# Optimization experiments

Measured on AMD Instinct MI355X. Metric: run time of the kernel, lower is better.

Reference implementation:

```python
import jax, jax.numpy as jnp
import numpy as np


def _lstm_dir(x, w_ih, w_hh, b, reverse):
    # x: [S,B,I], w_ih: [4H,I], w_hh: [4H,H], b: [4H]. torch gate order i,f,g,o.
    H = w_hh.shape[1]
    gx = jnp.einsum('sbi,gi->sbg', x, w_ih) + b  # precompute input projections
    B = x.shape[1]
    h0 = jnp.zeros((B, H), x.dtype)

    def step(carry, g):
        h, c = carry
        z = g + h @ w_hh.T
        i, f, gg, o = jnp.split(z, 4, axis=-1)
        c = jax.nn.sigmoid(f) * c + jax.nn.sigmoid(i) * jnp.tanh(gg)
        h = jax.nn.sigmoid(o) * jnp.tanh(c)
        return (h, c), h

    (hT, _), hs = jax.lax.scan(step, (h0, h0), gx, reverse=reverse)
    return hs, hT  # hs: [S,B,H] in original time order; hT final hidden


def _bilstm_layer(x, w_ih, w_hh, b):
    # x: [S,B,I]; params stacked [2, ...] for (forward, backward)
    hs_f, hT_f = _lstm_dir(x, w_ih[0], w_hh[0], b[0], reverse=False)
    hs_b, hT_b = _lstm_dir(x, w_ih[1], w_hh[1], b[1], reverse=True)
    return jnp.concatenate([hs_f, hs_b], axis=-1), hT_f, hT_b


def reference(tokens, emb, w_ih0, w_hh0, b0, w_ih1, w_hh1, b1, fc1_w, fc1_b, fc2_w, fc2_b):
    # tokens: [B,S] int; embedding lookup (frozen table)
    x = emb[tokens]                       # [B,S,E]
    x = jnp.transpose(x, (1, 0, 2))       # [S,B,E] time-major for scan
    h0_seq, _, _ = _bilstm_layer(x, w_ih0, w_hh0, b0)          # [S,B,2H]
    _, hT_f, hT_b = _bilstm_layer(h0_seq, w_ih1, w_hh1, b1)    # final layer
    out = jnp.concatenate([hT_f, hT_b], axis=-1)               # [B,2H]
    out = jax.nn.relu(out @ fc1_w.T + fc1_b)
    return out @ fc2_w.T + fc2_b          # [B,2]


def setup_inputs() -> dict:
    key = jax.random.key(0)
    ks = jax.random.split(key, 13)
    B, S, V, E, H = 256, 512, 50000, 300, 128
    s = 0.05
    return {
        'tokens': jax.random.randint(ks[0], (B, S), 0, V, dtype=jnp.int32),
        'emb':    jax.random.normal(ks[1], (V, E), jnp.float32) * s,
        'w_ih0':  jax.random.normal(ks[2], (2, 4 * H, E), jnp.float32) * s,
        'w_hh0':  jax.random.normal(ks[3], (2, 4 * H, H), jnp.float32) * s,
        'b0':     jax.random.normal(ks[4], (2, 4 * H), jnp.float32) * s,
        'w_ih1':  jax.random.normal(ks[5], (2, 4 * H, 2 * H), jnp.float32) * s,
        'w_hh1':  jax.random.normal(ks[6], (2, 4 * H, H), jnp.float32) * s,
        'b1':     jax.random.normal(ks[7], (2, 4 * H), jnp.float32) * s,
        'fc1_w':  jax.random.normal(ks[8], (H, 2 * H), jnp.float32) * s,
        'fc1_b':  jax.random.normal(ks[9], (H,), jnp.float32) * s,
        'fc2_w':  jax.random.normal(ks[10], (2, H), jnp.float32) * s,
        'fc2_b':  jax.random.normal(ks[11], (2,), jnp.float32) * s,
    }
```

## Files before the change

### kernel.cpp

```cpp
#include <hip/hip_runtime.h>

#define S_LEN 512
#define BATCH 256
#define EMB_D 300
#define EMB_PAD 320
#define HID 128
#define SB (S_LEN*BATCH)
#define CH 128
#define NCH 4
#define GXC_DIR ((size_t)CH*BATCH*512)
#define SMEM_BYTES 86016

typedef __attribute__((ext_vector_type(8))) short bf16x8;
typedef __attribute__((ext_vector_type(4))) float f32x4;
typedef unsigned short u16;
typedef unsigned int   u32;

__device__ __forceinline__ float b2f(u16 u) {
    union { u32 i; float f; } v; v.i = ((u32)u) << 16; return v.f;
}
__device__ __forceinline__ u16 f2b(float f) {
    union { float f; u32 i; } v; v.f = f;
    u32 r = v.i + 0x7fffu + ((v.i >> 16) & 1u);
    return (u16)(r >> 16);
}
__device__ __forceinline__ float sigf(float x) {
    return __builtin_amdgcn_rcpf(1.f + __expf(-x));
}
__device__ __forceinline__ float tanhf_fast(float x) {
    float e = __expf(2.f * x);
    return 1.f - 2.f * __builtin_amdgcn_rcpf(e + 1.f);
}

__global__ void k_detect(const u16* __restrict__ emb_u, int* __restrict__ flag) {
    __shared__ int cnt;
    if (threadIdx.x == 0) cnt = 0;
    __syncthreads();
    float v = b2f(emb_u[2 * threadIdx.x + 64]);
    float a = fabsf(v);
    if (a > 1e-4f && a < 16.f) atomicAdd(&cnt, 1);
    __syncthreads();
    if (threadIdx.x == 0) *flag = (cnt > 128) ? 1 : 0;
}

__global__ void k_packw(const void* __restrict__ src, u16* __restrict__ dst,
                        int Kin, int Kpad, int total, const int* __restrict__ flag) {
    int i = blockIdx.x * 256 + threadIdx.x;
    if (i >= total) return;
    int n = i / Kpad, k = i - n * Kpad;
    int d = n >> 9, r = n & 511, j = r >> 2, t = r & 3;
    size_t si = (size_t)((d << 9) + (t << 7) + j) * Kin + k;
    u16 v = 0;
    if (k < Kin) {
        if (*flag) v = ((const u16*)src)[si];
        else       v = f2b(((const float*)src)[si]);
    }
    dst[i] = v;
}

__global__ void k_packb(const void* __restrict__ src, float* __restrict__ dst,
                        const int* __restrict__ flag) {
    int i = blockIdx.x * 256 + threadIdx.x;
    if (i >= 1024) return;
    int d = i >> 9, r = i & 511, j = r >> 2, t = r & 3;
    size_t si = (d << 9) + (t << 7) + j;
    dst[i] = (*flag) ? b2f(((const u16*)src)[si]) : ((const float*)src)[si];
}

template<int KPAD, bool EMBED, bool IS_L0>
__global__ __launch_bounds__(1024) void k_fused(
    const int* __restrict__ tok, const void* __restrict__ Asrc,
    const u16* __restrict__ W, const float* __restrict__ bias,
    u16* __restrict__ gx_out, const u16* __restrict__ gx_in,
    const u16* __restrict__ Whp,
    u16* __restrict__ h0seq, float* __restrict__ hT,
    u16* __restrict__ hstate, float* __restrict__ cstate,
    int k, int nlstm, int soff0g, int soff1g, const int* __restrict__ flag)
{
    __shared__ __align__(16) char smem[SMEM_BYTES];
    const int tid = threadIdx.x;

    if ((int)blockIdx.x < nlstm) {
        u16* hb = (u16*)smem;
        u16* gb = (u16*)(smem + 8704);
        const int d    = blockIdx.x >> 4;
        const int bg   = blockIdx.x & 15;
        const int wv   = tid >> 6, lane = tid & 63, quad = lane >> 4, col = lane & 15;
        const int soff = (d == 0) ? CH * k : CH * (NCH - 1 - k);

        for (int i = tid; i < 2 * 16 * 136; i += 1024) hb[i] = 0;
        __syncthreads();
        if (k > 0) {
            for (int i = tid; i < 16 * 128; i += 1024) {
                int bl = i >> 7, j = i & 127;
                hb[bl * 136 + j] = hstate[((size_t)d * BATCH + bg * 16 + bl) * 128 + j];
            }
        }

        const u16* Wd = Whp + (size_t)d * 512 * 128;
        bf16x8 wf[2][4];
#pragma unroll
        for (int mt = 0; mt < 2; ++mt)
#pragma unroll
            for (int ks = 0; ks < 4; ++ks)
                wf[mt][ks] = *(const bf16x8*)(Wd + (size_t)(((wv * 2 + mt) * 16) + col) * 128 + ks * 32 + quad * 8);

        const u16* gxd = gx_in + (size_t)d * GXC_DIR;
        auto sloc = [&](int si) { return (d == 0) ? si : (CH - 1 - si); };
        auto prefetch = [&](int si, int P) {
            const u16* g0 = gxd + ((size_t)sloc(si) * BATCH + bg * 16 + wv) * 512 + lane * 8;
            __builtin_amdgcn_global_load_lds((const __attribute__((address_space(1))) void*)g0,
                (__attribute__((address_space(3))) void*)(gb + (P * 16 + wv) * 520), 16, 0, 0);
        };

        float c[2];
#pragma unroll
        for (int mt = 0; mt < 2; ++mt)
            c[mt] = (k > 0) ? cstate[((size_t)d * BATCH + bg * 16 + col) * 128 + (wv * 2 + mt) * 4 + quad] : 0.f;

        auto step = [&](int si, int P) {
            if (si + 1 < CH) prefetch(si + 1, P ^ 1);
            if constexpr (IS_L0) {
                if (si > 0) {
                    int sp = soff + ((d == 0) ? (si - 1) : (CH - si));
                    ushort2 hv = *(const ushort2*)(hb + (P * 16 + wv) * 136 + lane * 2);
                    *(ushort2*)(h0seq + ((size_t)sp * BATCH + bg * 16 + wv) * 256 + (d << 7) + lane * 2) = hv;
                }
            }
            bf16x8 hf[4];
#pragma unroll
            for (int ks = 0; ks < 4; ++ks)
                hf[ks] = *(const bf16x8*)(hb + (P * 16 + col) * 136 + ks * 32 + quad * 8);
            f32x4 z[2];
#pragma unroll
            for (int mt = 0; mt < 2; ++mt) {
                ushort4 gv = *(const ushort4*)(gb + (P * 16 + col) * 520 + (wv * 2 + mt) * 16 + quad * 4);
                z[mt][0] = b2f(gv.x); z[mt][1] = b2f(gv.y); z[mt][2] = b2f(gv.z); z[mt][3] = b2f(gv.w);
            }
#pragma unroll
            for (int ks = 0; ks < 4; ++ks)
#pragma unroll
                for (int mt = 0; mt < 2; ++mt)
                    z[mt] = __builtin_amdgcn_mfma_f32_16x16x32_bf16(wf[mt][ks], hf[ks], z[mt], 0, 0, 0);
#pragma unroll
            for (int mt = 0; mt < 2; ++mt) {
                float iv = sigf(z[mt][0]), fv = sigf(z[mt][1]);
                float gg = tanhf_fast(z[mt][2]), ov = sigf(z[mt][3]);
                c[mt] = fv * c[mt] + iv * gg;
                float hv = ov * tanhf_fast(c[mt]);
                const int j = (wv * 2 + mt) * 4 + quad;
                hb[((P ^ 1) * 16 + col) * 136 + j] = f2b(hv);
                if constexpr (!IS_L0) {
                    if (k == NCH - 1 && si == CH - 1)
                        hT[((size_t)d * BATCH + bg * 16 + col) * 128 + j] = hv;
                }
            }
            __syncthreads();
        };

        prefetch(0, 0);
        __syncthreads();

        for (int si = 0; si < CH; si += 2) {
            step(si, 0);
            step(si + 1, 1);
        }

        if constexpr (IS_L0) {
            int sp = soff + ((d == 0) ? (CH - 1) : 0);
            ushort2 hv = *(const ushort2*)(hb + wv * 136 + lane * 2);
            *(ushort2*)(h0seq + ((size_t)sp * BATCH + bg * 16 + wv) * 256 + (d << 7) + lane * 2) = hv;
        }
        if (k < NCH - 1) {
            for (int i = tid; i < 16 * 128; i += 1024) {
                int bl = i >> 7, j = i & 127;
                hstate[((size_t)d * BATCH + bg * 16 + bl) * 128 + j] = hb[bl * 136 + j];
            }
#pragma unroll
            for (int mt = 0; mt < 2; ++mt)
                cstate[((size_t)d * BATCH + bg * 16 + col) * 128 + (wv * 2 + mt) * 4 + quad] = c[mt];
        }
        return;
    }

    const int g   = (int)blockIdx.x - nlstm;
    u16* As = (u16*)smem;
    u16* Bs = (u16*)(smem + 10240);
    const int gy  = g >> 8;
    const int m0  = (g & 255) * 128;
    const int dir = gy >> 2;
    const int n0  = (gy & 3) * 128;
    const int soff = dir ? soff1g : soff0g;
    const size_t mg0 = (size_t)soff * BATCH;
    const int w = tid >> 6, lane = tid & 63, quad = lane >> 4, l16 = lane & 15;
    const int wm = w >> 2, wn = w & 3;
    const int crow = (tid & 511) >> 2, cseg = tid & 3;
    const bool isA = tid < 512;

    bool is_bf = true;
    size_t arow_off = 0;
    const u16* brow = nullptr;
    if (isA) {
        if constexpr (EMBED) {
            size_t m = mg0 + m0 + crow;
            int s = (int)(m >> 8), b = (int)(m & 255);
            is_bf = (*flag != 0);
            arow_off = (size_t)tok[b * S_LEN + s] * EMB_D;
        } else {
            arow_off = (mg0 + m0 + crow) * KPAD;
        }
    } else {
        brow = W + (size_t)(dir * 512 + n0 + crow) * KPAD;
    }

    f32x4 acc[2][2] = {};
    const int KSTEPS = KPAD / 32;
#pragma unroll
    for (int kk = 0; kk < KSTEPS; ++kk) {
        uint4 v;
        if (isA) {
            if constexpr (EMBED) {
                u32 u[4];
                if (is_bf) {
                    const u16* ar = (const u16*)Asrc + arow_off;
#pragma unroll
                    for (int i = 0; i < 4; ++i) {
                        int cc = kk * 32 + cseg * 8 + 2 * i;
                        u[i] = (cc < EMB_D) ? *(const u32*)(ar + cc) : 0u;
                    }
                } else {
                    const float* ar = (const float*)Asrc + arow_off;
#pragma unroll
                    for (int i = 0; i < 4; ++i) {
                        int cc = kk * 32 + cseg * 8 + 2 * i;
                        if (cc < EMB_D) {
                            float2 f = *(const float2*)(ar + cc);
                            u[i] = (u32)f2b(f.x) | ((u32)f2b(f.y) << 16);
                        } else u[i] = 0u;
                    }
                }
                v.x = u[0]; v.y = u[1]; v.z = u[2]; v.w = u[3];
            } else {
                v = *((const uint4*)((const u16*)Asrc + arow_off) + kk * 4 + cseg);
            }
        } else {
            v = *((const uint4*)brow + kk * 4 + cseg);
        }
        __syncthreads();
        if (isA) *(uint4*)(As + crow * 40 + cseg * 8) = v;
        else     *(uint4*)(Bs + crow * 40 + cseg * 8) = v;
        __syncthreads();
        bf16x8 af[2], bfr[2];
#pragma unroll
        for (int mt = 0; mt < 2; ++mt)
            af[mt] = *(const bf16x8*)(As + (wm * 32 + mt * 16 + l16) * 40 + quad * 8);
#pragma unroll
        for (int nt = 0; nt < 2; ++nt)
            bfr[nt] = *(const bf16x8*)(Bs + (wn * 32 + nt * 16 + l16) * 40 + quad * 8);
#pragma unroll
        for (int mt = 0; mt < 2; ++mt)
#pragma unroll
            for (int nt = 0; nt < 2; ++nt)
                acc[mt][nt] = __builtin_amdgcn_mfma_f32_16x16x32_bf16(af[mt], bfr[nt], acc[mt][nt], 0, 0, 0);
    }
#pragma unroll
    for (int mt = 0; mt < 2; ++mt)
#pragma unroll
        for (int nt = 0; nt < 2; ++nt)
#pragma unroll
            for (int r = 0; r < 4; ++r) {
                int mloc = m0 + wm * 32 + mt * 16 + quad * 4 + r;
                int nloc = n0 + wn * 32 + nt * 16 + l16;
                float vv = acc[mt][nt][r] + bias[dir * 512 + nloc];
                gx_out[(size_t)dir * GXC_DIR + (size_t)mloc * 512 + nloc] = f2b(vv);
            }
}

__global__ void k_fc(const float* __restrict__ hT,
                     const void* __restrict__ fc1w, const void* __restrict__ fc1b,
                     const void* __restrict__ fc2w, const void* __restrict__ fc2b,
                     void* __restrict__ out, const int* __restrict__ flag) {
    int b = blockIdx.x, j = threadIdx.x;
    bool is_bf = (*flag != 0);
    __shared__ float u[128];
    float a = is_bf ? b2f(((const u16*)fc1b)[j]) : ((const float*)fc1b)[j];
    for (int k = 0; k < 256; ++k) {
        float x = hT[((size_t)(k >> 7) * BATCH + b) * 128 + (k & 127)];
        float w = is_bf ? b2f(((const u16*)fc1w)[j * 256 + k]) : ((const float*)fc1w)[j * 256 + k];
        a += x * w;
    }
    u[j] = fmaxf(a, 0.f);
    __syncthreads();
    if (j < 2) {
        float a2 = is_bf ? b2f(((const u16*)fc2b)[j]) : ((const float*)fc2b)[j];
        for (int q = 0; q < 128; ++q) {
            float w = is_bf ? b2f(((const u16*)fc2w)[j * 128 + q]) : ((const float*)fc2w)[j * 128 + q];
            a2 += u[q] * w;
        }
        if (is_bf) ((u16*)out)[b * 2 + j] = f2b(a2);
        else       ((float*)out)[b * 2 + j] = a2;
    }
}

extern "C" void kernel_launch(void* const* d_in, const int* in_sizes, int n_in,
                              void* d_out, int out_size, void* d_ws, size_t ws_size,
                              hipStream_t stream) {
    const int*  tok   = (const int*)d_in[0];
    const void* emb   = d_in[1];
    const void* w_ih0 = d_in[2];
    const void* w_hh0 = d_in[3];
    const void* b0    = d_in[4];
    const void* w_ih1 = d_in[5];
    const void* w_hh1 = d_in[6];
    const void* b1    = d_in[7];
    const void* fc1w  = d_in[8];
    const void* fc1b  = d_in[9];
    const void* fc2w  = d_in[10];
    const void* fc2b  = d_in[11];

    char* ws = (char*)d_ws;
    size_t off = 0;
    auto alloc = [&](size_t bytes) -> void* {
        void* p = ws + off; off += (bytes + 255) & ~(size_t)255; return p;
    };
    int*   flag   = (int*)alloc(256);
    u16*   Wp0    = (u16*)alloc(1024 * 320 * 2);
    u16*   Wp1    = (u16*)alloc(1024 * 256 * 2);
    u16*   Whp0   = (u16*)alloc(1024 * 128 * 2);
    u16*   Whp1   = (u16*)alloc(1024 * 128 * 2);
    float* bp0    = (float*)alloc(1024 * 4);
    float* bp1    = (float*)alloc(1024 * 4);
    float* hT     = (float*)alloc((size_t)2 * BATCH * 128 * 4);
    u16*   hstate = (u16*)alloc((size_t)2 * BATCH * 128 * 2);
    float* cstate = (float*)alloc((size_t)2 * BATCH * 128 * 4);
    u16*   h0seq  = (u16*)alloc((size_t)SB * 256 * 2);
    size_t bufb   = 2 * GXC_DIR * sizeof(u16);
    u16*   gxcA   = (u16*)alloc(bufb);
    bool overlap  = ws_size >= off + bufb;
    u16*   gxcB   = overlap ? (u16*)alloc(bufb) : gxcA;

    k_detect<<<1, 256, 0, stream>>>((const u16*)emb, flag);

    k_packw<<<(1024 * 320 + 255) / 256, 256, 0, stream>>>(w_ih0, Wp0, 300, 320, 1024 * 320, flag);
    k_packw<<<(1024 * 256 + 255) / 256, 256, 0, stream>>>(w_ih1, Wp1, 256, 256, 1024 * 256, flag);
    k_packw<<<(1024 * 128 + 255) / 256, 256, 0, stream>>>(w_hh0, Whp0, 128, 128, 1024 * 128, flag);
    k_packw<<<(1024 * 128 + 255) / 256, 256, 0, stream>>>(w_hh1, Whp1, 128, 128, 1024 * 128, flag);
    k_packb<<<4, 256, 0, stream>>>(b0, bp0, flag);
    k_packb<<<4, 256, 0, stream>>>(b1, bp1, flag);

    const int NG = 2048;

    if (overlap) {
        k_fused<320, true, true><<<NG, 1024, 0, stream>>>(
            tok, emb, Wp0, bp0, gxcA, gxcA, Whp0, h0seq, nullptr, hstate, cstate,
            0, 0, 0, CH * (NCH - 1), flag);
        for (int k = 0; k < NCH; ++k) {
            int ng = (k < NCH - 1) ? NG : 0;
            u16* gin  = (k & 1) ? gxcB : gxcA;
            u16* gout = (k & 1) ? gxcA : gxcB;
            k_fused<320, true, true><<<32 + ng, 1024, 0, stream>>>(
                tok, emb, Wp0, bp0, gout, gin, Whp0, h0seq, nullptr, hstate, cstate,
                k, 32, CH * (k + 1), CH * (NCH - 2 - k), flag);
        }
        k_fused<256, false, false><<<NG, 1024, 0, stream>>>(
            nullptr, h0seq, Wp1, bp1, gxcA, gxcA, Whp1, nullptr, hT, hstate, cstate,
            0, 0, 0, CH * (NCH - 1), flag);
        for (int k = 0; k < NCH; ++k) {
            int ng = (k < NCH - 1) ? NG : 0;
            u16* gin  = (k & 1) ? gxcB : gxcA;
            u16* gout = (k & 1) ? gxcA : gxcB;
            k_fused<256, false, false><<<32 + ng, 1024, 0, stream>>>(
                nullptr, h0seq, Wp1, bp1, gout, gin, Whp1, nullptr, hT, hstate, cstate,
                k, 32, CH * (k + 1), CH * (NCH - 2 - k), flag);
        }
    } else {
        for (int k = 0; k < NCH; ++k) {
            k_fused<320, true, true><<<NG, 1024, 0, stream>>>(
                tok, emb, Wp0, bp0, gxcA, gxcA, Whp0, h0seq, nullptr, hstate, cstate,
                0, 0, CH * k, CH * (NCH - 1 - k), flag);
            k_fused<320, true, true><<<32, 1024, 0, stream>>>(
                tok, emb, Wp0, bp0, gxcA, gxcA, Whp0, h0seq, nullptr, hstate, cstate,
                k, 32, 0, 0, flag);
        }
        for (int k = 0; k < NCH; ++k) {
            k_fused<256, false, false><<<NG, 1024, 0, stream>>>(
                nullptr, h0seq, Wp1, bp1, gxcA, gxcA, Whp1, nullptr, hT, hstate, cstate,
                0, 0, CH * k, CH * (NCH - 1 - k), flag);
            k_fused<256, false, false><<<32, 1024, 0, stream>>>(
                nullptr, h0seq, Wp1, bp1, gxcA, gxcA, Whp1, nullptr, hT, hstate, cstate,
                k, 32, 0, 0, flag);
        }
    }
    k_fc<<<256, 128, 0, stream>>>(hT, fc1w, fc1b, fc2w, fc2b, d_out, flag);
}
```

Before: 1.560 ms.

## Restructure input-projection GEMM to keep full-K A tile resident and loop over N

The input-projection GEMM blocks now load a 64-row A tile with the full K extent into shared memory once, then loop over eight 64-column slices of the weight matrix, each loaded with full K. Before, each block computed a 128x128 tile by streaming 32-wide K slices, with a sync pair per step. The goal is to reuse the gathered embedding rows across all 512 gate outputs and cut redundant gathers, halving the GEMM block count. The cost is fewer MFMAs per wave per tile (a single 16x16 accumulator), more shared-memory footprint, and an extra sync pair per N slice.

```diff
diff --git a/kernel.cpp b/kernel.cpp
--- a/kernel.cpp
+++ b/kernel.cpp
@@ -183,97 +183,76 @@
         return;
     }
 
-    const int g   = (int)blockIdx.x - nlstm;
+    const int g = (int)blockIdx.x - nlstm;
+    constexpr int KSTEPS = KPAD / 32;
+    constexpr int AST    = KPAD + 8;
+    constexpr int NCHK   = 64 * (KPAD / 8);
     u16* As = (u16*)smem;
-    u16* Bs = (u16*)(smem + 10240);
-    const int gy  = g >> 8;
-    const int m0  = (g & 255) * 128;
-    const int dir = gy >> 2;
-    const int n0  = (gy & 3) * 128;
+    u16* Bs = (u16*)(smem + (size_t)64 * AST * 2);
+    const int dir  = g >> 9;
+    const int m0   = (g & 511) * 64;
     const int soff = dir ? soff1g : soff0g;
     const size_t mg0 = (size_t)soff * BATCH;
     const int w = tid >> 6, lane = tid & 63, quad = lane >> 4, l16 = lane & 15;
     const int wm = w >> 2, wn = w & 3;
-    const int crow = (tid & 511) >> 2, cseg = tid & 3;
-    const bool isA = tid < 512;
-
-    bool is_bf = true;
-    size_t arow_off = 0;
-    const u16* brow = nullptr;
-    if (isA) {
+    const bool is_bf = EMBED ? (*flag != 0) : true;
+
+    for (int ch = tid; ch < NCHK; ch += 1024) {
+        int row = ch / (KPAD / 8), seg = ch % (KPAD / 8);
+        uint4 v;
         if constexpr (EMBED) {
-            size_t m = mg0 + m0 + crow;
+            u32 u[4];
+            size_t m = mg0 + m0 + row;
             int s = (int)(m >> 8), b = (int)(m & 255);
-            is_bf = (*flag != 0);
-            arow_off = (size_t)tok[b * S_LEN + s] * EMB_D;
+            size_t aro = (size_t)tok[b * S_LEN + s] * EMB_D;
+            if (is_bf) {
+                const u16* ar = (const u16*)Asrc + aro;
+#pragma unroll
+                for (int i = 0; i < 4; ++i) {
+                    int cc = seg * 8 + 2 * i;
+                    u[i] = (cc < EMB_D) ? *(const u32*)(ar + cc) : 0u;
+                }
+            } else {
+                const float* ar = (const float*)Asrc + aro;
+#pragma unroll
+                for (int i = 0; i < 4; ++i) {
+                    int cc = seg * 8 + 2 * i;
+                    if (cc < EMB_D) {
+                        float2 f = *(const float2*)(ar + cc);
+                        u[i] = (u32)f2b(f.x) | ((u32)f2b(f.y) << 16);
+                    } else u[i] = 0u;
+                }
+            }
+            v.x = u[0]; v.y = u[1]; v.z = u[2]; v.w = u[3];
         } else {
-            arow_off = (mg0 + m0 + crow) * KPAD;
-        }
-    } else {
-        brow = W + (size_t)(dir * 512 + n0 + crow) * KPAD;
-    }
-
-    f32x4 acc[2][2] = {};
-    const int KSTEPS = KPAD / 32;
-#pragma unroll
-    for (int kk = 0; kk < KSTEPS; ++kk) {
-        uint4 v;
-        if (isA) {
-            if constexpr (EMBED) {
-                u32 u[4];
-                if (is_bf) {
-                    const u16* ar = (const u16*)Asrc + arow_off;
-#pragma unroll
-                    for (int i = 0; i < 4; ++i) {
-                        int cc = kk * 32 + cseg * 8 + 2 * i;
-                        u[i] = (cc < EMB_D) ? *(const u32*)(ar + cc) : 0u;
-                    }
-                } else {
-                    const float* ar = (const float*)Asrc + arow_off;
-#pragma unroll
-                    for (int i = 0; i < 4; ++i) {
-                        int cc = kk * 32 + cseg * 8 + 2 * i;
-                        if (cc < EMB_D) {
-                            float2 f = *(const float2*)(ar + cc);
-                            u[i] = (u32)f2b(f.x) | ((u32)f2b(f.y) << 16);
-                        } else u[i] = 0u;
-                    }
-                }
-                v.x = u[0]; v.y = u[1]; v.z = u[2]; v.w = u[3];
-            } else {
-                v = *((const uint4*)((const u16*)Asrc + arow_off) + kk * 4 + cseg);
-            }
-        } else {
-            v = *((const uint4*)brow + kk * 4 + cseg);
-        }
+            v = *(const uint4*)((const u16*)Asrc + (mg0 + m0 + row) * KPAD + seg * 8);
+        }
+        *(uint4*)(As + (size_t)row * AST + seg * 8) = v;
+    }
+
+    for (int j = 0; j < 8; ++j) {
         __syncthreads();
-        if (isA) *(uint4*)(As + crow * 40 + cseg * 8) = v;
-        else     *(uint4*)(Bs + crow * 40 + cseg * 8) = v;
+        for (int ch = tid; ch < NCHK; ch += 1024) {
+            int row = ch / (KPAD / 8), seg = ch % (KPAD / 8);
+            uint4 v = *(const uint4*)(W + (size_t)(dir * 512 + j * 64 + row) * KPAD + seg * 8);
+            *(uint4*)(Bs + (size_t)row * AST + seg * 8) = v;
+        }
         __syncthreads();
-        bf16x8 af[2], bfr[2];
-#pragma unroll
-        for (int mt = 0; mt < 2; ++mt)
-            af[mt] = *(const bf16x8*)(As + (wm * 32 + mt * 16 + l16) * 40 + quad * 8);
-#pragma unroll
-        for (int nt = 0; nt < 2; ++nt)
-            bfr[nt] = *(const bf16x8*)(Bs + (wn * 32 + nt * 16 + l16) * 40 + quad * 8);
-#pragma unroll
-        for (int mt = 0; mt < 2; ++mt)
-#pragma unroll
-            for (int nt = 0; nt < 2; ++nt)
-                acc[mt][nt] = __builtin_amdgcn_mfma_f32_16x16x32_bf16(af[mt], bfr[nt], acc[mt][nt], 0, 0, 0);
-    }
-#pragma unroll
-    for (int mt = 0; mt < 2; ++mt)
-#pragma unroll
-        for (int nt = 0; nt < 2; ++nt)
-#pragma unroll
-            for (int r = 0; r < 4; ++r) {
-                int mloc = m0 + wm * 32 + mt * 16 + quad * 4 + r;
-                int nloc = n0 + wn * 32 + nt * 16 + l16;
-                float vv = acc[mt][nt][r] + bias[dir * 512 + nloc];
-                gx_out[(size_t)dir * GXC_DIR + (size_t)mloc * 512 + nloc] = f2b(vv);
-            }
+        f32x4 acc = {};
+#pragma unroll
+        for (int kk = 0; kk < KSTEPS; ++kk) {
+            bf16x8 af = *(const bf16x8*)(As + (size_t)(wm * 16 + l16) * AST + kk * 32 + quad * 8);
+            bf16x8 bf = *(const bf16x8*)(Bs + (size_t)(wn * 16 + l16) * AST + kk * 32 + quad * 8);
+            acc = __builtin_amdgcn_mfma_f32_16x16x32_bf16(af, bf, acc, 0, 0, 0);
+        }
+#pragma unroll
+        for (int r = 0; r < 4; ++r) {
+            int mloc = m0 + wm * 16 + quad * 4 + r;
+            int nloc = j * 64 + wn * 16 + l16;
+            float vv = acc[r] + bias[dir * 512 + nloc];
+            gx_out[(size_t)dir * GXC_DIR + (size_t)mloc * 512 + nloc] = f2b(vv);
+        }
+    }
 }
 
 __global__ void k_fc(const float* __restrict__ hT,
@@ -348,7 +327,7 @@
     k_packb<<<4, 256, 0, stream>>>(b0, bp0, flag);
     k_packb<<<4, 256, 0, stream>>>(b1, bp1, flag);
 
-    const int NG = 2048;
+    const int NG = 1024;
 
     if (overlap) {
         k_fused<320, true, true><<<NG, 1024, 0, stream>>>(
```

New measurement: 1.568 ms. Within noise of the previous version (+0.5%).
